# Kernel optimization log

Hardware: AMD Instinct MI355X
Metric: run time of the kernel (lower is better)

Reference implementation:

```python
import jax, jax.numpy as jnp
import numpy as np

SL, BS, HS, FFN = 2048, 1, 512, 2048
E, TOP_K = 8, 2


def setup_inputs() -> dict:
    key = jax.random.key(0)
    k_x, k_w, k_i, k_w1, k_w2 = jax.random.split(key, 5)
    x = jax.random.normal(k_x, (SL, BS, HS), dtype=jnp.float32)
    expert_weights = jax.random.uniform(k_w, (SL * BS, TOP_K), dtype=jnp.float32)
    expert_indices = jax.random.randint(k_i, (SL * BS, TOP_K), 0, E, dtype=jnp.int32)
    # grouped expert MLP params (megablocks GroupedMLP, regular type, no bias)
    w1 = jax.random.normal(k_w1, (E, HS, FFN), dtype=jnp.float32) * (HS ** -0.5)
    w2 = jax.random.normal(k_w2, (E, FFN, HS), dtype=jnp.float32) * (FFN ** -0.5)
    return {"x": x, "expert_weights": expert_weights, "expert_indices": expert_indices,
            "w1": w1, "w2": w2}


def reference(x, expert_weights, expert_indices, w1, w2):
    sl, bs, hs = x.shape
    n_tok = sl * bs
    xf = x.reshape(n_tok, hs)                      # [N, hs]
    ew = expert_weights.reshape(-1)                # [N*top_k]
    ei = expert_indices.reshape(-1)                # [N*top_k]

    # indices_and_bins: stable radix sort of assignments by expert id
    indices = jnp.argsort(ei)                      # stable in jax -> sorted assignment ids
    bin_ids = ei[indices]                          # sorted expert id per assignment

    # megablocks gather: row for assignment i is indices[i] // top_k
    rows = indices // TOP_K                        # [T]
    xg = xf[rows]                                  # [T, hs] expert-contiguous tokens

    # grouped GEMM expert MLP (dense masked loop over fixed expert count)
    outg = jnp.zeros_like(xg)
    for e in range(E):
        m = (bin_ids == e).astype(x.dtype)[:, None]
        h = jax.nn.gelu(xg @ w1[e], approximate=False)   # [T, ffn]
        outg = outg + m * (h @ w2[e])                    # [T, hs]

    # buffer.index_add_(0, E*input_indices + bin_ids, output.detach())
    buf_idx = E * rows + bin_ids
    buffer = jnp.zeros((n_tok * E, hs), x.dtype).at[buf_idx].add(
        jax.lax.stop_gradient(outg))

    # megablocks scatter: weighted combine back to token order
    y = jnp.zeros((n_tok, hs), x.dtype).at[rows].add(outg * ew[indices][:, None])
    return y.reshape(sl, bs, hs), buffer.reshape(n_tok, E, hs)
```

## Files before the change

kernel.cpp:

```cpp
#include <hip/hip_runtime.h>
#include <hip/hip_bf16.h>

#define NTOK 2048
#define TOPK 2
#define HS   512
#define FFN  2048
#define NE   8
#define TASSIGN (NTOK*TOPK)
#define PAD  5120
#define MAXT128 40
#define MAXT64  72

typedef __attribute__((ext_vector_type(8))) short bf16x8;
typedef __attribute__((ext_vector_type(8))) unsigned short u16x8;
typedef __attribute__((ext_vector_type(4))) float f32x4;

static const size_t OFF_XBF  = 0;
static const size_t OFF_W1T  = 2097152;
static const size_t OFF_W2T  = 18874368;
static const size_t OFF_H    = 35651584;
static const size_t OFF_OUTV = 56623104;
static const size_t OFF_RT   = 67108864;
static const size_t OFF_HROF = 67129344;
static const size_t OFF_TE128= 67145728;
static const size_t OFF_TR128= 67145888;
static const size_t OFF_TE64 = 67146048;
static const size_t OFF_TR64 = 67146336;

__device__ __forceinline__ unsigned short f2bf(float f) {
    union { __hip_bfloat16 h; unsigned short u; } v;
    v.h = __float2bfloat16(f);
    return v.u;
}

__device__ __forceinline__ float bf2f(unsigned short u) {
    union { unsigned int i; float f; } v;
    v.i = ((unsigned int)u) << 16;
    return v.f;
}

__device__ __forceinline__ int swz(int r, int byte_off) {
    return byte_off ^ ((r & 7) << 4);
}

__device__ __forceinline__ float gelu_fast(float x) {
    float z2 = x * fmaf(0.0713548162726f, x * x, 1.5957691216057f);
    float e = __expf(z2);
    return x - __fdividef(x, e + 1.0f);
}

#define GLOAD16(gsrc, ldst) \
    __builtin_amdgcn_global_load_lds((const __attribute__((address_space(1))) void*)(gsrc), \
                                     (__attribute__((address_space(3))) void*)(ldst), 16, 0, 0)

__device__ __forceinline__ void dev_tr2(const float* __restrict__ in,
                                        unsigned short* __restrict__ out,
                                        int R, int C, int e, int rb, int cb,
                                        int tid, unsigned short* t ) {
    const float* ip = in + (size_t)e * R * C + (size_t)rb * C + cb;
    unsigned short* op = out + (size_t)e * C * R + (size_t)cb * R + rb;
    int r = tid >> 3, c8 = (tid & 7) * 8;
    float4 v0 = *(const float4*)(ip + (size_t)r * C + c8);
    float4 v1 = *(const float4*)(ip + (size_t)r * C + c8 + 4);
    ushort4 lo, hi;
    lo.x = f2bf(v0.x); lo.y = f2bf(v0.y); lo.z = f2bf(v0.z); lo.w = f2bf(v0.w);
    hi.x = f2bf(v1.x); hi.y = f2bf(v1.y); hi.z = f2bf(v1.z); hi.w = f2bf(v1.w);
    *(ushort4*)(t + r * 72 + c8)     = lo;
    *(ushort4*)(t + r * 72 + c8 + 4) = hi;
    __syncthreads();
    int c = tid >> 2, r8 = (tid & 3) * 8;
    ushort4 a, b;
    a.x = t[(r8 + 0) * 72 + c]; a.y = t[(r8 + 1) * 72 + c];
    a.z = t[(r8 + 2) * 72 + c]; a.w = t[(r8 + 3) * 72 + c];
    b.x = t[(r8 + 4) * 72 + c]; b.y = t[(r8 + 5) * 72 + c];
    b.z = t[(r8 + 6) * 72 + c]; b.w = t[(r8 + 7) * 72 + c];
    *(ushort4*)(op + (size_t)c * R + r8)     = a;
    *(ushort4*)(op + (size_t)c * R + r8 + 4) = b;
}

__global__ __launch_bounds__(256) void k_prep(
        const float* __restrict__ x, const float* __restrict__ w1,
        const float* __restrict__ w2, const int* __restrict__ ei,
        unsigned short* __restrict__ xbf, unsigned short* __restrict__ w1T,
        unsigned short* __restrict__ w2T,
        int* __restrict__ rowtok, int* __restrict__ hrof,
        int* __restrict__ te128, int* __restrict__ tr128,
        int* __restrict__ te64, int* __restrict__ tr64) {
    __shared__ unsigned short tsh[32 * 72];
    int b = blockIdx.x;
    int tid = threadIdx.x;
    if (b == 0) {
        __shared__ int cnt[NE], offpad[NE], cur[NE];
        for (int i = tid; i < PAD; i += 256) rowtok[i] = 0;
        if (tid < NE) cnt[tid] = 0;
        __syncthreads();
        for (int a = tid; a < TASSIGN; a += 256) atomicAdd(&cnt[ei[a]], 1);
        __syncthreads();
        if (tid == 0) {
            int o = 0, t1 = 0, t2 = 0;
            for (int e = 0; e < NE; e++) {
                offpad[e] = o; cur[e] = 0;
                for (int r = 0; r < cnt[e]; r += 128) { te128[t1] = e; tr128[t1] = o + r; t1++; }
                for (int r = 0; r < cnt[e]; r += 64)  { te64[t2]  = e; tr64[t2]  = o + r; t2++; }
                o += (cnt[e] + 127) / 128 * 128;
            }
            for (; t1 < MAXT128; t1++) te128[t1] = -1;
            for (; t2 < MAXT64;  t2++) te64[t2]  = -1;
        }
        __syncthreads();
        for (int a = tid; a < TASSIGN; a += 256) {
            int e = ei[a];
            int r = atomicAdd(&cur[e], 1);
            int hr = offpad[e] + r;
            rowtok[hr] = a >> 1;
            hrof[a] = hr;
        }
    } else if (b < 1 + 512) {
        int i = ((b - 1) * 256 + tid) * 8;
        float4 v0 = *(const float4*)(x + i);
        float4 v1 = *(const float4*)(x + i + 4);
        u16x8 o;
        o[0] = f2bf(v0.x); o[1] = f2bf(v0.y); o[2] = f2bf(v0.z); o[3] = f2bf(v0.w);
        o[4] = f2bf(v1.x); o[5] = f2bf(v1.y); o[6] = f2bf(v1.z); o[7] = f2bf(v1.w);
        *(u16x8*)(xbf + i) = o;
    } else if (b < 1 + 512 + 4096) {
        int blk = b - 513;
        int e = blk >> 9, u = blk & 511;
        dev_tr2(w1, w1T, HS, FFN, e, (u >> 5) * 32, (u & 31) * 64, tid, tsh);
    } else {
        int blk = b - 4609;
        int e = blk >> 9, u = blk & 511;
        dev_tr2(w2, w2T, FFN, HS, e, (u >> 3) * 32, (u & 7) * 64, tid, tsh);
    }
}

template<int BM, int BN, int KFULL, int KLOC, bool G1>
__global__ __launch_bounds__(256) void k_gemm(
        const unsigned short* __restrict__ A,
        const unsigned short* __restrict__ B,
        unsigned short* __restrict__ outp,
        const int* __restrict__ rowtok,
        const int* __restrict__ te, const int* __restrict__ tr, int N) {
    constexpr int MI = BM / 32, NJ = BN / 32;
    constexpr int PA = BM / 32, PB = BN / 32;
    constexpr int ABYTES = BM * 64 * 2, BBYTES = BN * 64 * 2;
    constexpr int NSTEP = KLOC / 64;
    static_assert(NSTEP % 2 == 0 && NSTEP >= 4, "even steps >= 4");

    int mt = blockIdx.y;
    int e = te[mt];
    if (e < 0) return;
    int hr0 = tr[mt];
    int ct = blockIdx.x;
    int kz = blockIdx.z;
    int k0 = kz * KLOC;

    __shared__ int4 ldsv[(2 * (ABYTES + BBYTES)) / 16];
    char* A0 = (char*)ldsv;
    char* A1 = A0 + ABYTES;
    char* B0 = A1 + ABYTES;
    char* B1 = B0 + BBYTES;

    int tid = threadIdx.x;
    int lane = tid & 63, wave = tid >> 6;
    int wm = wave >> 1, wn = wave & 1;

    const char* asrc[PA];
    const char* bsrc[PB];
    int adoff[PA], bdoff[PB];
#pragma unroll
    for (int p = 0; p < PA; p++) {
        int idx = p * 256 + tid;
        int r = idx >> 3, c8 = idx & 7;
        int c8s = c8 ^ (r & 7);
        size_t row = G1 ? (size_t)rowtok[hr0 + r] : (size_t)(hr0 + r);
        asrc[p] = (const char*)(A + row * KFULL + k0) + c8s * 16;
        adoff[p] = (p * 256 + wave * 64) * 16;
    }
#pragma unroll
    for (int p = 0; p < PB; p++) {
        int idx = p * 256 + tid;
        int r = idx >> 3, c8 = idx & 7;
        int c8s = c8 ^ (r & 7);
        bsrc[p] = (const char*)(B + ((size_t)e * N + (size_t)ct * BN + r) * KFULL + k0) + c8s * 16;
        bdoff[p] = (p * 256 + wave * 64) * 16;
    }

    f32x4 acc[MI][NJ] = {};

    auto stage = [&](char* Ad, char* Bd, int s) {
        int kb = s * 128;
#pragma unroll
        for (int p = 0; p < PA; p++) GLOAD16(asrc[p] + kb, Ad + adoff[p]);
#pragma unroll
        for (int p = 0; p < PB; p++) GLOAD16(bsrc[p] + kb, Bd + bdoff[p]);
    };
    auto compute = [&](const char* As, const char* Bs) {
#pragma unroll
        for (int kk = 0; kk < 64; kk += 32) {
            bf16x8 af[MI], bfv[NJ];
#pragma unroll
            for (int i = 0; i < MI; i++) {
                int ar = wm * (BM / 2) + i * 16 + (lane & 15);
                af[i] = *(const bf16x8*)(As + swz(ar, ar * 128 + kk * 2 + (lane >> 4) * 16));
            }
#pragma unroll
            for (int j = 0; j < NJ; j++) {
                int bc = wn * (BN / 2) + j * 16 + (lane & 15);
                bfv[j] = *(const bf16x8*)(Bs + swz(bc, bc * 128 + kk * 2 + (lane >> 4) * 16));
            }
#pragma unroll
            for (int i = 0; i < MI; i++)
#pragma unroll
                for (int j = 0; j < NJ; j++)
                    acc[i][j] = __builtin_amdgcn_mfma_f32_16x16x32_bf16(af[i], bfv[j], acc[i][j], 0, 0, 0);
        }
    };
    auto waitv_lps = [&]() {
        if constexpr (PA + PB == 6)      { asm volatile("s_waitcnt vmcnt(6)" ::: "memory"); }
        else if constexpr (PA + PB == 4) { asm volatile("s_waitcnt vmcnt(4)" ::: "memory"); }
        else                             { asm volatile("s_waitcnt vmcnt(0)" ::: "memory"); }
    };
    auto waitv0 = [&]() { asm volatile("s_waitcnt vmcnt(0)" ::: "memory"); };
    auto waitlgkm = [&]() { asm volatile("s_waitcnt lgkmcnt(0)" ::: "memory"); };
    auto bar = [&]() {
        __builtin_amdgcn_sched_barrier(0);
        __builtin_amdgcn_s_barrier();
        __builtin_amdgcn_sched_barrier(0);
        asm volatile("" ::: "memory");
    };

    stage(A0, B0, 0);
    stage(A1, B1, 1);
#pragma unroll 1
    for (int s = 0; s + 2 < NSTEP; s += 2) {
        waitv_lps(); bar();
        compute(A0, B0);
        waitlgkm(); bar();
        stage(A0, B0, s + 2);
        waitv_lps(); bar();
        compute(A1, B1);
        waitlgkm(); bar();
        if (s + 3 < NSTEP) stage(A1, B1, s + 3);
    }
    waitv_lps(); bar();
    compute(A0, B0);
    waitv0(); bar();
    compute(A1, B1);

    if constexpr (G1) {
#pragma unroll
        for (int i = 0; i < MI; i++)
#pragma unroll
            for (int j = 0; j < NJ; j++)
#pragma unroll
                for (int q = 0; q < 4; q++) {
                    int row = hr0 + wm * (BM / 2) + i * 16 + (lane >> 4) * 4 + q;
                    int col = ct * BN + wn * (BN / 2) + j * 16 + (lane & 15);
                    outp[(size_t)row * N + col] = f2bf(gelu_fast(acc[i][j][q]));
                }
    } else {
        unsigned short* O = outp + (size_t)kz * PAD * HS;
#pragma unroll
        for (int i = 0; i < MI; i++)
#pragma unroll
            for (int j = 0; j < NJ; j++)
#pragma unroll
                for (int q = 0; q < 4; q++) {
                    int row = hr0 + wm * (BM / 2) + i * 16 + (lane >> 4) * 4 + q;
                    int col = ct * BN + wn * (BN / 2) + j * 16 + (lane & 15);
                    O[(size_t)row * N + col] = f2bf(acc[i][j][q]);
                }
    }
}

__global__ __launch_bounds__(256) void k_combine(
        const unsigned short* __restrict__ outv, const int* __restrict__ ei,
        const float* __restrict__ ew, const int* __restrict__ hrof,
        float* __restrict__ y, float* __restrict__ buf) {
    constexpr size_t SPLIT = (size_t)PAD * HS;
    int g = blockIdx.x * 256 + threadIdx.x;
    int t = g >> 6, c8 = g & 63;
    int a0 = 2 * t, a1 = a0 + 1;
    int h0 = hrof[a0], h1 = hrof[a1];
    u16x8 q0a = *(const u16x8*)(outv + (size_t)h0 * HS + c8 * 8);
    u16x8 q0b = *(const u16x8*)(outv + SPLIT + (size_t)h0 * HS + c8 * 8);
    u16x8 q1a = *(const u16x8*)(outv + (size_t)h1 * HS + c8 * 8);
    u16x8 q1b = *(const u16x8*)(outv + SPLIT + (size_t)h1 * HS + c8 * 8);
    float w0 = ew[a0], w1 = ew[a1];
    float o0[8], o1[8], yy[8];
#pragma unroll
    for (int k = 0; k < 8; k++) {
        o0[k] = bf2f(q0a[k]) + bf2f(q0b[k]);
        o1[k] = bf2f(q1a[k]) + bf2f(q1b[k]);
        yy[k] = w0 * o0[k] + w1 * o1[k];
    }
    float* yp = y + (size_t)t * HS + c8 * 8;
    *(float4*)(yp)     = make_float4(yy[0], yy[1], yy[2], yy[3]);
    *(float4*)(yp + 4) = make_float4(yy[4], yy[5], yy[6], yy[7]);
    int e0 = ei[a0], e1 = ei[a1];
    float* bt = buf + (size_t)t * (NE * HS) + c8 * 8;
#pragma unroll
    for (int e = 0; e < NE; e++) {
        float v[8];
#pragma unroll
        for (int k = 0; k < 8; k++)
            v[k] = (e == e0 ? o0[k] : 0.0f) + (e == e1 ? o1[k] : 0.0f);
        float* be = bt + (size_t)e * HS;
        *(float4*)(be)     = make_float4(v[0], v[1], v[2], v[3]);
        *(float4*)(be + 4) = make_float4(v[4], v[5], v[6], v[7]);
    }
}

extern "C" void kernel_launch(void* const* d_in, const int* in_sizes, int n_in,
                              void* d_out, int out_size, void* d_ws, size_t ws_size,
                              hipStream_t stream) {
    const float* x  = (const float*)d_in[0];
    const float* ew = (const float*)d_in[1];
    const int*   ei = (const int*)d_in[2];
    const float* w1 = (const float*)d_in[3];
    const float* w2 = (const float*)d_in[4];

    char* ws = (char*)d_ws;
    unsigned short* xbf  = (unsigned short*)(ws + OFF_XBF);
    unsigned short* w1T  = (unsigned short*)(ws + OFF_W1T);
    unsigned short* w2T  = (unsigned short*)(ws + OFF_W2T);
    unsigned short* Hb   = (unsigned short*)(ws + OFF_H);
    unsigned short* outv = (unsigned short*)(ws + OFF_OUTV);
    int*            rowtok = (int*)(ws + OFF_RT);
    int*            hrof   = (int*)(ws + OFF_HROF);
    int*            te128  = (int*)(ws + OFF_TE128);
    int*            tr128  = (int*)(ws + OFF_TR128);
    int*            te64   = (int*)(ws + OFF_TE64);
    int*            tr64   = (int*)(ws + OFF_TR64);

    float* y   = (float*)d_out;
    float* buf = (float*)d_out + (size_t)NTOK * HS;

    k_prep<<<1 + 512 + 4096 + 4096, 256, 0, stream>>>(
        x, w1, w2, ei, xbf, w1T, w2T, rowtok, hrof, te128, tr128, te64, tr64);
    k_gemm<128, 64, HS, HS, true><<<dim3(FFN / 64, MAXT128), 256, 0, stream>>>(
        xbf, w1T, Hb, rowtok, te128, tr128, FFN);
    k_gemm<64, 64, FFN, FFN / 2, false><<<dim3(HS / 64, MAXT64, 2), 256, 0, stream>>>(
        Hb, w2T, outv, rowtok, te64, tr64, HS);
    k_combine<<<NTOK * HS / 8 / 256, 256, 0, stream>>>(
        outv, ei, ew, hrof, y, buf);
}
```

Baseline: 86.18 us.

## Triple-buffer LDS tiles in grouped GEMM with one barrier per k-step

```diff
diff --git a/kernel.cpp b/kernel.cpp
--- a/kernel.cpp
+++ b/kernel.cpp
@@ -145,7 +145,7 @@
     constexpr int PA = BM / 32, PB = BN / 32;
     constexpr int ABYTES = BM * 64 * 2, BBYTES = BN * 64 * 2;
     constexpr int NSTEP = KLOC / 64;
-    static_assert(NSTEP % 2 == 0 && NSTEP >= 4, "even steps >= 4");
+    static_assert(NSTEP >= 3, "steps >= 3");
 
     int mt = blockIdx.y;
     int e = te[mt];
@@ -155,11 +155,9 @@
     int kz = blockIdx.z;
     int k0 = kz * KLOC;
 
-    __shared__ int4 ldsv[(2 * (ABYTES + BBYTES)) / 16];
-    char* A0 = (char*)ldsv;
-    char* A1 = A0 + ABYTES;
-    char* B0 = A1 + ABYTES;
-    char* B1 = B0 + BBYTES;
+    __shared__ int4 ldsv[(3 * (ABYTES + BBYTES)) / 16];
+    char* Abase = (char*)ldsv;
+    char* Bbase = Abase + 3 * ABYTES;
 
     int tid = threadIdx.x;
     int lane = tid & 63, wave = tid >> 6;
@@ -222,7 +220,6 @@
         else                             { asm volatile("s_waitcnt vmcnt(0)" ::: "memory"); }
     };
     auto waitv0 = [&]() { asm volatile("s_waitcnt vmcnt(0)" ::: "memory"); };
-    auto waitlgkm = [&]() { asm volatile("s_waitcnt lgkmcnt(0)" ::: "memory"); };
     auto bar = [&]() {
         __builtin_amdgcn_sched_barrier(0);
         __builtin_amdgcn_s_barrier();
@@ -230,23 +227,19 @@
         asm volatile("" ::: "memory");
     };
 
-    stage(A0, B0, 0);
-    stage(A1, B1, 1);
-#pragma unroll 1
-    for (int s = 0; s + 2 < NSTEP; s += 2) {
-        waitv_lps(); bar();
-        compute(A0, B0);
-        waitlgkm(); bar();
-        stage(A0, B0, s + 2);
-        waitv_lps(); bar();
-        compute(A1, B1);
-        waitlgkm(); bar();
-        if (s + 3 < NSTEP) stage(A1, B1, s + 3);
-    }
-    waitv_lps(); bar();
-    compute(A0, B0);
-    waitv0(); bar();
-    compute(A1, B1);
+    stage(Abase + 0 * ABYTES, Bbase + 0 * BBYTES, 0);
+    stage(Abase + 1 * ABYTES, Bbase + 1 * BBYTES, 1);
+#pragma unroll
+    for (int s = 0; s < NSTEP; s++) {
+        if (s == NSTEP - 1) { waitv0(); } else { waitv_lps(); }
+        bar();
+        if (s + 2 < NSTEP) {
+            int m2 = (s + 2) % 3;
+            stage(Abase + m2 * ABYTES, Bbase + m2 * BBYTES, s + 2);
+        }
+        int m = s % 3;
+        compute(Abase + m * ABYTES, Bbase + m * BBYTES);
+    }
 
     if constexpr (G1) {
 #pragma unroll
```

Result: no change. 86.85 us (+0.8%).

## Overlap w2 transpose-convert with first expert GEMM in a fused launch

Applied to the files above, without the earlier changes.

```diff
diff --git a/kernel.cpp b/kernel.cpp
--- a/kernel.cpp
+++ b/kernel.cpp
@@ -56,7 +56,7 @@
 __device__ __forceinline__ void dev_tr2(const float* __restrict__ in,
                                         unsigned short* __restrict__ out,
                                         int R, int C, int e, int rb, int cb,
-                                        int tid, unsigned short* t ) {
+                                        int tid, unsigned short* t) {
     const float* ip = in + (size_t)e * R * C + (size_t)rb * C + cb;
     unsigned short* op = out + (size_t)e * C * R + (size_t)cb * R + rb;
     int r = tid >> 3, c8 = (tid & 7) * 8;
@@ -80,9 +80,8 @@
 
 __global__ __launch_bounds__(256) void k_prep(
         const float* __restrict__ x, const float* __restrict__ w1,
-        const float* __restrict__ w2, const int* __restrict__ ei,
+        const int* __restrict__ ei,
         unsigned short* __restrict__ xbf, unsigned short* __restrict__ w1T,
-        unsigned short* __restrict__ w2T,
         int* __restrict__ rowtok, int* __restrict__ hrof,
         int* __restrict__ te128, int* __restrict__ tr128,
         int* __restrict__ te64, int* __restrict__ tr64) {
@@ -123,45 +122,55 @@
         o[0] = f2bf(v0.x); o[1] = f2bf(v0.y); o[2] = f2bf(v0.z); o[3] = f2bf(v0.w);
         o[4] = f2bf(v1.x); o[5] = f2bf(v1.y); o[6] = f2bf(v1.z); o[7] = f2bf(v1.w);
         *(u16x8*)(xbf + i) = o;
-    } else if (b < 1 + 512 + 4096) {
+    } else {
         int blk = b - 513;
-        int e = blk >> 9, u = blk & 511;
-        dev_tr2(w1, w1T, HS, FFN, e, (u >> 5) * 32, (u & 31) * 64, tid, tsh);
-    } else {
-        int blk = b - 4609;
-        int e = blk >> 9, u = blk & 511;
-        dev_tr2(w2, w2T, FFN, HS, e, (u >> 3) * 32, (u & 7) * 64, tid, tsh);
-    }
-}
-
-template<int BM, int BN, int KFULL, int KLOC, bool G1>
-__global__ __launch_bounds__(256) void k_gemm(
+        int e = blk >> 9, rem = blk & 511;
+        dev_tr2(w1, w1T, HS, FFN, e, (rem >> 5) * 32, (rem & 31) * 64, tid, tsh);
+    }
+}
+
+__global__ __launch_bounds__(256) void k_g1w2t(
         const unsigned short* __restrict__ A,
         const unsigned short* __restrict__ B,
-        unsigned short* __restrict__ outp,
+        unsigned short* __restrict__ Hout,
         const int* __restrict__ rowtok,
-        const int* __restrict__ te, const int* __restrict__ tr, int N) {
-    constexpr int MI = BM / 32, NJ = BN / 32;
-    constexpr int PA = BM / 32, PB = BN / 32;
+        const int* __restrict__ te, const int* __restrict__ tr,
+        const float* __restrict__ w2, unsigned short* __restrict__ w2T) {
+    constexpr int BM = 128, BN = 64, K = HS, N = FFN;
+    constexpr int MI = 4, NJ = 2, PA = 4, PB = 2;
     constexpr int ABYTES = BM * 64 * 2, BBYTES = BN * 64 * 2;
-    constexpr int NSTEP = KLOC / 64;
-    static_assert(NSTEP % 2 == 0 && NSTEP >= 4, "even steps >= 4");
-
-    int mt = blockIdx.y;
+    constexpr int NSTEP = K / 64;
+
+    __shared__ int4 ldsv[(2 * (ABYTES + BBYTES)) / 16];
+    int b = blockIdx.x;
+    int tid = threadIdx.x;
+
+    if (b % 6 == 0) {
+        unsigned short* tsh = (unsigned short*)ldsv;
+        int tb = b / 6;
+#pragma unroll 1
+        for (int i = 0; i < 16; ++i) {
+            if (i) __syncthreads();
+            int t = tb * 16 + i;
+            int e2 = t >> 9;
+            int rem = t & 511;
+            dev_tr2(w2, w2T, FFN, HS, e2, (rem >> 3) * 32, (rem & 7) * 64, tid, tsh);
+        }
+        return;
+    }
+
+    int bb = b - 1 - b / 6;
+    int ct = bb & 31;
+    int mt = bb >> 5;
     int e = te[mt];
     if (e < 0) return;
     int hr0 = tr[mt];
-    int ct = blockIdx.x;
-    int kz = blockIdx.z;
-    int k0 = kz * KLOC;
-
-    __shared__ int4 ldsv[(2 * (ABYTES + BBYTES)) / 16];
+
     char* A0 = (char*)ldsv;
     char* A1 = A0 + ABYTES;
     char* B0 = A1 + ABYTES;
     char* B1 = B0 + BBYTES;
 
-    int tid = threadIdx.x;
     int lane = tid & 63, wave = tid >> 6;
     int wm = wave >> 1, wn = wave & 1;
 
@@ -173,8 +182,8 @@
         int idx = p * 256 + tid;
         int r = idx >> 3, c8 = idx & 7;
         int c8s = c8 ^ (r & 7);
-        size_t row = G1 ? (size_t)rowtok[hr0 + r] : (size_t)(hr0 + r);
-        asrc[p] = (const char*)(A + row * KFULL + k0) + c8s * 16;
+        size_t row = (size_t)rowtok[hr0 + r];
+        asrc[p] = (const char*)(A + row * K) + c8s * 16;
         adoff[p] = (p * 256 + wave * 64) * 16;
     }
 #pragma unroll
@@ -182,7 +191,7 @@
         int idx = p * 256 + tid;
         int r = idx >> 3, c8 = idx & 7;
         int c8s = c8 ^ (r & 7);
-        bsrc[p] = (const char*)(B + ((size_t)e * N + (size_t)ct * BN + r) * KFULL + k0) + c8s * 16;
+        bsrc[p] = (const char*)(B + ((size_t)e * N + (size_t)ct * BN + r) * K) + c8s * 16;
         bdoff[p] = (p * 256 + wave * 64) * 16;
     }
 
@@ -216,11 +225,7 @@
                     acc[i][j] = __builtin_amdgcn_mfma_f32_16x16x32_bf16(af[i], bfv[j], acc[i][j], 0, 0, 0);
         }
     };
-    auto waitv_lps = [&]() {
-        if constexpr (PA + PB == 6)      { asm volatile("s_waitcnt vmcnt(6)" ::: "memory"); }
-        else if constexpr (PA + PB == 4) { asm volatile("s_waitcnt vmcnt(4)" ::: "memory"); }
-        else                             { asm volatile("s_waitcnt vmcnt(0)" ::: "memory"); }
-    };
+    auto waitv_lps = [&]() { asm volatile("s_waitcnt vmcnt(6)" ::: "memory"); };
     auto waitv0 = [&]() { asm volatile("s_waitcnt vmcnt(0)" ::: "memory"); };
     auto waitlgkm = [&]() { asm volatile("s_waitcnt lgkmcnt(0)" ::: "memory"); };
     auto bar = [&]() {
@@ -248,30 +253,141 @@
     waitv0(); bar();
     compute(A1, B1);
 
-    if constexpr (G1) {
-#pragma unroll
-        for (int i = 0; i < MI; i++)
-#pragma unroll
-            for (int j = 0; j < NJ; j++)
-#pragma unroll
-                for (int q = 0; q < 4; q++) {
-                    int row = hr0 + wm * (BM / 2) + i * 16 + (lane >> 4) * 4 + q;
-                    int col = ct * BN + wn * (BN / 2) + j * 16 + (lane & 15);
-                    outp[(size_t)row * N + col] = f2bf(gelu_fast(acc[i][j][q]));
-                }
-    } else {
-        unsigned short* O = outp + (size_t)kz * PAD * HS;
-#pragma unroll
-        for (int i = 0; i < MI; i++)
-#pragma unroll
-            for (int j = 0; j < NJ; j++)
-#pragma unroll
-                for (int q = 0; q < 4; q++) {
-                    int row = hr0 + wm * (BM / 2) + i * 16 + (lane >> 4) * 4 + q;
-                    int col = ct * BN + wn * (BN / 2) + j * 16 + (lane & 15);
-                    O[(size_t)row * N + col] = f2bf(acc[i][j][q]);
-                }
-    }
+#pragma unroll
+    for (int i = 0; i < MI; i++)
+#pragma unroll
+        for (int j = 0; j < NJ; j++)
+#pragma unroll
+            for (int q = 0; q < 4; q++) {
+                int row = hr0 + wm * (BM / 2) + i * 16 + (lane >> 4) * 4 + q;
+                int col = ct * BN + wn * (BN / 2) + j * 16 + (lane & 15);
+                Hout[(size_t)row * N + col] = f2bf(gelu_fast(acc[i][j][q]));
+            }
+}
+
+template<int BM, int BN, int KFULL, int KLOC>
+__global__ __launch_bounds__(256) void k_gemm2(
+        const unsigned short* __restrict__ A,
+        const unsigned short* __restrict__ B,
+        unsigned short* __restrict__ outp,
+        const int* __restrict__ te, const int* __restrict__ tr, int N) {
+    constexpr int MI = BM / 32, NJ = BN / 32;
+    constexpr int PA = BM / 32, PB = BN / 32;
+    constexpr int ABYTES = BM * 64 * 2, BBYTES = BN * 64 * 2;
+    constexpr int NSTEP = KLOC / 64;
+    static_assert(NSTEP % 2 == 0 && NSTEP >= 4, "even steps >= 4");
+
+    int mt = blockIdx.y;
+    int e = te[mt];
+    if (e < 0) return;
+    int hr0 = tr[mt];
+    int ct = blockIdx.x;
+    int kz = blockIdx.z;
+    int k0 = kz * KLOC;
+
+    __shared__ int4 ldsv[(2 * (ABYTES + BBYTES)) / 16];
+    char* A0 = (char*)ldsv;
+    char* A1 = A0 + ABYTES;
+    char* B0 = A1 + ABYTES;
+    char* B1 = B0 + BBYTES;
+
+    int tid = threadIdx.x;
+    int lane = tid & 63, wave = tid >> 6;
+    int wm = wave >> 1, wn = wave & 1;
+
+    const char* asrc[PA];
+    const char* bsrc[PB];
+    int adoff[PA], bdoff[PB];
+#pragma unroll
+    for (int p = 0; p < PA; p++) {
+        int idx = p * 256 + tid;
+        int r = idx >> 3, c8 = idx & 7;
+        int c8s = c8 ^ (r & 7);
+        asrc[p] = (const char*)(A + (size_t)(hr0 + r) * KFULL + k0) + c8s * 16;
+        adoff[p] = (p * 256 + wave * 64) * 16;
+    }
+#pragma unroll
+    for (int p = 0; p < PB; p++) {
+        int idx = p * 256 + tid;
+        int r = idx >> 3, c8 = idx & 7;
+        int c8s = c8 ^ (r & 7);
+        bsrc[p] = (const char*)(B + ((size_t)e * N + (size_t)ct * BN + r) * KFULL + k0) + c8s * 16;
+        bdoff[p] = (p * 256 + wave * 64) * 16;
+    }
+
+    f32x4 acc[MI][NJ] = {};
+
+    auto stage = [&](char* Ad, char* Bd, int s) {
+        int kb = s * 128;
+#pragma unroll
+        for (int p = 0; p < PA; p++) GLOAD16(asrc[p] + kb, Ad + adoff[p]);
+#pragma unroll
+        for (int p = 0; p < PB; p++) GLOAD16(bsrc[p] + kb, Bd + bdoff[p]);
+    };
+    auto compute = [&](const char* As, const char* Bs) {
+#pragma unroll
+        for (int kk = 0; kk < 64; kk += 32) {
+            bf16x8 af[MI], bfv[NJ];
+#pragma unroll
+            for (int i = 0; i < MI; i++) {
+                int ar = wm * (BM / 2) + i * 16 + (lane & 15);
+                af[i] = *(const bf16x8*)(As + swz(ar, ar * 128 + kk * 2 + (lane >> 4) * 16));
+            }
+#pragma unroll
+            for (int j = 0; j < NJ; j++) {
+                int bc = wn * (BN / 2) + j * 16 + (lane & 15);
+                bfv[j] = *(const bf16x8*)(Bs + swz(bc, bc * 128 + kk * 2 + (lane >> 4) * 16));
+            }
+#pragma unroll
+            for (int i = 0; i < MI; i++)
+#pragma unroll
+                for (int j = 0; j < NJ; j++)
+                    acc[i][j] = __builtin_amdgcn_mfma_f32_16x16x32_bf16(af[i], bfv[j], acc[i][j], 0, 0, 0);
+        }
+    };
+    auto waitv_lps = [&]() {
+        if constexpr (PA + PB == 6)      { asm volatile("s_waitcnt vmcnt(6)" ::: "memory"); }
+        else if constexpr (PA + PB == 4) { asm volatile("s_waitcnt vmcnt(4)" ::: "memory"); }
+        else                             { asm volatile("s_waitcnt vmcnt(0)" ::: "memory"); }
+    };
+    auto waitv0 = [&]() { asm volatile("s_waitcnt vmcnt(0)" ::: "memory"); };
+    auto waitlgkm = [&]() { asm volatile("s_waitcnt lgkmcnt(0)" ::: "memory"); };
+    auto bar = [&]() {
+        __builtin_amdgcn_sched_barrier(0);
+        __builtin_amdgcn_s_barrier();
+        __builtin_amdgcn_sched_barrier(0);
+        asm volatile("" ::: "memory");
+    };
+
+    stage(A0, B0, 0);
+    stage(A1, B1, 1);
+#pragma unroll 1
+    for (int s = 0; s + 2 < NSTEP; s += 2) {
+        waitv_lps(); bar();
+        compute(A0, B0);
+        waitlgkm(); bar();
+        stage(A0, B0, s + 2);
+        waitv_lps(); bar();
+        compute(A1, B1);
+        waitlgkm(); bar();
+        if (s + 3 < NSTEP) stage(A1, B1, s + 3);
+    }
+    waitv_lps(); bar();
+    compute(A0, B0);
+    waitv0(); bar();
+    compute(A1, B1);
+
+    unsigned short* O = outp + (size_t)kz * PAD * HS;
+#pragma unroll
+    for (int i = 0; i < MI; i++)
+#pragma unroll
+        for (int j = 0; j < NJ; j++)
+#pragma unroll
+            for (int q = 0; q < 4; q++) {
+                int row = hr0 + wm * (BM / 2) + i * 16 + (lane >> 4) * 4 + q;
+                int col = ct * BN + wn * (BN / 2) + j * 16 + (lane & 15);
+                O[(size_t)row * N + col] = f2bf(acc[i][j][q]);
+            }
 }
 
 __global__ __launch_bounds__(256) void k_combine(
@@ -337,12 +453,12 @@
     float* y   = (float*)d_out;
     float* buf = (float*)d_out + (size_t)NTOK * HS;
 
-    k_prep<<<1 + 512 + 4096 + 4096, 256, 0, stream>>>(
-        x, w1, w2, ei, xbf, w1T, w2T, rowtok, hrof, te128, tr128, te64, tr64);
-    k_gemm<128, 64, HS, HS, true><<<dim3(FFN / 64, MAXT128), 256, 0, stream>>>(
-        xbf, w1T, Hb, rowtok, te128, tr128, FFN);
-    k_gemm<64, 64, FFN, FFN / 2, false><<<dim3(HS / 64, MAXT64, 2), 256, 0, stream>>>(
-        Hb, w2T, outv, rowtok, te64, tr64, HS);
+    k_prep<<<1 + 512 + 4096, 256, 0, stream>>>(
+        x, w1, ei, xbf, w1T, rowtok, hrof, te128, tr128, te64, tr64);
+    k_g1w2t<<<1536, 256, 0, stream>>>(
+        xbf, w1T, Hb, rowtok, te128, tr128, w2, w2T);
+    k_gemm2<64, 64, FFN, FFN / 2><<<dim3(HS / 64, MAXT64, 2), 256, 0, stream>>>(
+        Hb, w2T, outv, te64, tr64, HS);
     k_combine<<<NTOK * HS / 8 / 256, 256, 0, stream>>>(
         outv, ei, ew, hrof, y, buf);
 }
```

Result: slower. 94.24 us (+9.4%).
